# Kernel tuning notes

Measured on AMD Instinct MI355X. Metric: run time of the kernel, lower is better.

## Reference

```python
import jax, jax.numpy as jnp
import numpy as np

# Clebsch-Gordan coefficients in the real basis; l=1 components stored in (y,z,x) order
S2 = 1.0 / np.sqrt(2.0)
S3 = 1.0 / np.sqrt(3.0)
S6 = 1.0 / np.sqrt(6.0)
_C2 = np.zeros((5, 3, 3), np.float32)
_C2[0, 2, 0] = _C2[0, 0, 2] = S2          # ~ xy
_C2[1, 0, 1] = _C2[1, 1, 0] = S2          # ~ yz
_C2[2, 1, 1] = 2.0 * S6                   # ~ 2z^2 - x^2 - y^2
_C2[2, 2, 2] = -S6
_C2[2, 0, 0] = -S6
_C2[3, 2, 1] = _C2[3, 1, 2] = S2          # ~ xz
_C2[4, 2, 2] = S2                          # ~ x^2 - y^2
_C2[4, 0, 0] = -S2
C2 = jnp.asarray(_C2)

N0, N1 = 64, 32        # multiplicities of input 0e / 1o irreps
CUTOFF = 5.0


def basis_functions(pos):
    """pos [N,3] -> (scalars [N,64], l=1 features [N,32,3])."""
    r = jnp.linalg.norm(pos, axis=-1, keepdims=True) + 1e-9        # [N,1]
    d = pos[:, (1, 2, 0)] / r                                       # unit dir, (y,z,x) order
    c0 = jnp.linspace(0.0, CUTOFF, N0, dtype=pos.dtype)
    c1 = jnp.linspace(0.0, CUTOFF, N1, dtype=pos.dtype)
    f0 = jnp.exp(-4.0 * (r - c0) ** 2)                              # [N,64] gaussian RBF
    f1 = jnp.exp(-4.0 * (r - c1) ** 2)                              # [N,32]
    x1 = f1[:, :, None] * d[:, None, :]                             # [N,32,3]
    return f0, x1


def lin_l(x, W):
    # channel mixing within one irrep block; preserves the m axis if present
    if x.ndim == 2:
        return x @ W
    return jnp.einsum('ncm,cd->ndm', x, W)


def tensor_product(a0, a1, b0, b1):
    """Full uvw CG tensor product of (64x0 + 32x1) x (64x0 + 32x1)."""
    N = a0.shape[0]
    # l=0 outputs: 0x0->0 and 1x1->0
    p000 = jnp.einsum('na,nb->nab', a0, b0).reshape(N, -1)                 # [N,4096]
    p110 = jnp.einsum('nam,nbm->nab', a1, b1).reshape(N, -1) * S3          # [N,1024]
    t0 = jnp.concatenate([p000, p110], axis=1)                             # [N,5120]
    # l=1 outputs: 0x1->1, 1x0->1, 1x1->1 (cross product)
    p011 = (a0[:, :, None, None] * b1[:, None, :, :]).reshape(N, -1, 3)    # [N,2048,3]
    p101 = (a1[:, :, None, :] * b0[:, None, :, None]).reshape(N, -1, 3)    # [N,2048,3]
    p111 = (jnp.cross(a1[:, :, None, :], b1[:, None, :, :]) * S2).reshape(N, -1, 3)
    t1 = jnp.concatenate([p011, p101, p111], axis=1)                       # [N,5120,3]
    # l=2 output: 1x1->2 via CG tensor
    t2 = jnp.einsum('nai,nbj,mij->nabm', a1, b1, C2).reshape(N, -1, 5)     # [N,1024,5]
    return t0, t1, t2


def setup_inputs() -> dict:
    key = jax.random.key(0)
    ks = jax.random.split(key, 10)
    N = 4096
    def w(k, i, o):
        return jax.random.normal(k, (i, o), jnp.float32) / np.sqrt(i)
    return {
        'positions': jax.random.normal(ks[0], (N, 3), jnp.float32) * 2.0,
        'W1_0': w(ks[1], 64, 64),
        'W1_1': w(ks[2], 32, 32),
        'W2_0': w(ks[3], 64, 64),
        'W2_1': w(ks[4], 32, 32),
        'W3_0': w(ks[5], 5120, 64),
        'W3_1': w(ks[6], 5120, 32),
        'W3_2': w(ks[7], 1024, 16),
        'W_out': w(ks[8], 240, 7),
        'b_out': jnp.zeros((7,), jnp.float32),
    }


def reference(positions, W1_0, W1_1, W2_0, W2_1, W3_0, W3_1, W3_2, W_out, b_out):
    f0, f1 = basis_functions(positions)                 # 64x0, 32x1
    a0, a1 = lin_l(f0, W1_0), lin_l(f1, W1_1)           # linear1
    b0, b1 = lin_l(f0, W2_0), lin_l(f1, W2_1)           # linear2
    t0, t1, t2 = tensor_product(a0, a1, b0, b1)         # 5120x0, 5120x1, 1024x2
    y0 = lin_l(t0, W3_0)                                # [N,64]
    y1 = lin_l(t1, W3_1)                                # [N,32,3]
    y2 = lin_l(t2, W3_2)                                # [N,16,5]
    N = y0.shape[0]
    feat = jnp.concatenate([y0, y1.reshape(N, -1), y2.reshape(N, -1)], axis=1)  # [N,240]
    return feat @ W_out + b_out                         # [N,7]
```

## Files before the change

### kernel.cpp

```cpp
#include <hip/hip_runtime.h>
#include <math.h>

#define NS2 0.70710678118654752440f
#define NS3 0.57735026918962576451f
#define NS6 0.40824829046386301636f

typedef _Float16 f16;
typedef _Float16 f16x8 __attribute__((ext_vector_type(8)));
typedef float    f32x4 __attribute__((ext_vector_type(4)));

#define GT_K    22528
#define UV_ROW  216
#define OFF_UV  157696

__global__ __launch_bounds__(256) void prep_kernel(
    const float* __restrict__ pos,
    const float* __restrict__ W1_0, const float* __restrict__ W1_1,
    const float* __restrict__ W2_0, const float* __restrict__ W2_1,
    const float* __restrict__ W3_0, const float* __restrict__ W3_1,
    const float* __restrict__ W3_2, const float* __restrict__ Wout,
    const float* __restrict__ bout,
    f16* __restrict__ wsh, float* __restrict__ out, int N)
{
    __shared__ float smem[3728];
    const int tid = threadIdx.x;

    if (blockIdx.x < 352) {
        float* s_wo  = smem;
        float* s_red = smem + 1680;
        for (int i = tid; i < 1680; i += 256) s_wo[i] = Wout[i];
        __syncthreads();
        const int kl = tid & 63, q = tid >> 6;
        const int k  = blockIdx.x * 64 + kl;
        float acc[7] = {0.f,0.f,0.f,0.f,0.f,0.f,0.f};
        if (k < 4096) {
            const float* wr = W3_0 + (size_t)k * 64;
            #pragma unroll
            for (int oo = 0; oo < 16; oo += 4) {
                int o = q*16 + oo;
                float4 wv = *(const float4*)(wr + o);
                const float* w0 = s_wo + o * 7;
                #pragma unroll
                for (int kk = 0; kk < 7; ++kk)
                    acc[kk] = fmaf(wv.x, w0[kk], fmaf(wv.y, w0[7+kk],
                              fmaf(wv.z, w0[14+kk], fmaf(wv.w, w0[21+kk], acc[kk]))));
            }
        } else if (k < 10240) {
            int it = k >> 6, s = it - 64, m = s >> 5, a2 = s & 31, l = k & 63;
            const float* wr = W3_1 + (size_t)(2048 + a2*64 + l) * 32;
            #pragma unroll
            for (int oo = 0; oo < 8; oo += 4) {
                int o = q*8 + oo;
                float4 wv = *(const float4*)(wr + o);
                const float* w0 = s_wo + (64 + o*3 + m) * 7;
                #pragma unroll
                for (int kk = 0; kk < 7; ++kk)
                    acc[kk] = fmaf(wv.x, w0[kk], fmaf(wv.y, w0[21+kk],
                              fmaf(wv.z, w0[42+kk], fmaf(wv.w, w0[63+kk], acc[kk]))));
            }
        } else {
            int it2 = (k - 10240) >> 5, l32 = k & 31;
            if (it2 < 32) {
                const float* wr = W3_0 + (size_t)(4096 + it2*32 + l32) * 64;
                #pragma unroll
                for (int oo = 0; oo < 16; oo += 4) {
                    int o = q*16 + oo;
                    float4 wv = *(const float4*)(wr + o);
                    const float* w0 = s_wo + o * 7;
                    #pragma unroll
                    for (int kk = 0; kk < 7; ++kk)
                        acc[kk] = fmaf(wv.x, w0[kk], fmaf(wv.y, w0[7+kk],
                                  fmaf(wv.z, w0[14+kk], fmaf(wv.w, w0[21+kk], acc[kk]))));
                }
            } else if (it2 < 224) {
                int t = it2 - 32, m = t >> 6, a = t & 63;
                const float* wr = W3_1 + (size_t)(a*32 + l32) * 32;
                #pragma unroll
                for (int oo = 0; oo < 8; oo += 4) {
                    int o = q*8 + oo;
                    float4 wv = *(const float4*)(wr + o);
                    const float* w0 = s_wo + (64 + o*3 + m) * 7;
                    #pragma unroll
                    for (int kk = 0; kk < 7; ++kk)
                        acc[kk] = fmaf(wv.x, w0[kk], fmaf(wv.y, w0[21+kk],
                                  fmaf(wv.z, w0[42+kk], fmaf(wv.w, w0[63+kk], acc[kk]))));
                }
            } else {
                int t = it2 - 224, m = t >> 5, a = t & 31;
                const float* wr = W3_2 + (size_t)(a*32 + l32) * 16;
                int o = q*4;
                float4 wv = *(const float4*)(wr + o);
                const float* w0 = s_wo + (160 + o*5 + m) * 7;
                #pragma unroll
                for (int kk = 0; kk < 7; ++kk)
                    acc[kk] = fmaf(wv.x, w0[kk], fmaf(wv.y, w0[35+kk],
                              fmaf(wv.z, w0[70+kk], fmaf(wv.w, w0[105+kk], acc[kk]))));
            }
        }
        #pragma unroll
        for (int r = 0; r < 7; ++r) s_red[(q*64 + kl)*8 + r] = acc[r];
        __syncthreads();
        if (tid < 64) {
            #pragma unroll
            for (int r = 0; r < 7; ++r) {
                float v = s_red[(      tid)*8 + r] + s_red[( 64 + tid)*8 + r]
                        + s_red[(128 + tid)*8 + r] + s_red[(192 + tid)*8 + r];
                wsh[(size_t)r * GT_K + blockIdx.x*64 + tid] = (f16)v;
            }
        }
        return;
    }

    float* s_f0 = smem;
    float* s_f1 = smem + 512;
    const int g8   = blockIdx.x - 352;
    const int base = g8 * 8;
    f16* uv = wsh + OFF_UV;
    {
        int d = tid & 63;
        #pragma unroll
        for (int jj = 0; jj < 2; ++jj) {
            int j = (tid >> 6) + jj * 4;
            int n = base + j;
            float px = pos[n*3+0], py = pos[n*3+1], pz = pos[n*3+2];
            float r  = sqrtf(px*px + py*py + pz*pz) + 1e-9f;
            float t0 = r - (5.0f/63.0f) * (float)d;
            s_f0[j*64 + d] = __expf(-4.f * t0 * t0);
        }
        {
            int j = tid >> 5, d1 = tid & 31;
            int n = base + j;
            float px = pos[n*3+0], py = pos[n*3+1], pz = pos[n*3+2];
            float r  = sqrtf(px*px + py*py + pz*pz) + 1e-9f;
            float t1 = r - (5.0f/31.0f) * (float)d1;
            s_f1[j*32 + d1] = __expf(-4.f * t1 * t1);
        }
        if (tid < 8) {
            int n = base + tid;
            float px = pos[n*3+0], py = pos[n*3+1], pz = pos[n*3+2];
            float r  = sqrtf(px*px + py*py + pz*pz) + 1e-9f;
            float iv = 1.0f / r;
            float d0 = py*iv, d1 = pz*iv, d2 = px*iv;
            f16* row = uv + (size_t)n * UV_ROW;
            row[192+0] = (f16)d0;
            row[192+1] = (f16)d1;
            row[192+2] = (f16)d2;
            row[192+3] = (f16)(NS3 * (d0*d0 + d1*d1 + d2*d2));
            row[192+4] = (f16)(2.f*NS2*d2*d0);
            row[192+5] = (f16)(2.f*NS2*d0*d1);
            row[192+6] = (f16)(NS6*(2.f*d1*d1 - d2*d2 - d0*d0));
            row[192+7] = (f16)(2.f*NS2*d2*d1);
            row[192+8] = (f16)(NS2*(d2*d2 - d0*d0));
            row[201]   = (f16)1.0f;
        }
        if (tid < 56) out[base*7 + tid] = bout[tid % 7];
    }
    __syncthreads();
    {
        int c = tid & 63, jb = tid >> 6;
        float aa0 = 0.f, aa1 = 0.f, ba0 = 0.f, ba1 = 0.f;
        const float* wa = W1_0 + c;
        const float* wb = W2_0 + c;
        #pragma unroll 4
        for (int d = 0; d < 64; ++d) {
            float wav = wa[d*64], wbv = wb[d*64];
            float fA = s_f0[jb*64 + d], fB = s_f0[(jb+4)*64 + d];
            aa0 = fmaf(fA, wav, aa0);  aa1 = fmaf(fB, wav, aa1);
            ba0 = fmaf(fA, wbv, ba0);  ba1 = fmaf(fB, wbv, ba1);
        }
        uv[(size_t)(base+jb  )*UV_ROW +      c] = (f16)aa0;
        uv[(size_t)(base+jb+4)*UV_ROW +      c] = (f16)aa1;
        uv[(size_t)(base+jb  )*UV_ROW + 96 + c] = (f16)ba0;
        uv[(size_t)(base+jb+4)*UV_ROW + 96 + c] = (f16)ba1;

        int c1 = tid & 31, j8 = tid >> 5;
        float aA = 0.f, aB = 0.f;
        const float* wA = W1_1 + c1;
        const float* wB = W2_1 + c1;
        #pragma unroll 4
        for (int d = 0; d < 32; ++d) {
            float f = s_f1[j8*32 + d];
            aA = fmaf(f, wA[d*32], aA);
            aB = fmaf(f, wB[d*32], aB);
        }
        uv[(size_t)(base+j8)*UV_ROW +  64 + c1] = (f16)aA;
        uv[(size_t)(base+j8)*UV_ROW + 160 + c1] = (f16)aB;
    }
}

__global__ __launch_bounds__(256) void main_kernel(
    const f16* __restrict__ wsh, float* __restrict__ out, int N)
{
    __shared__ f16 s_g[2][8][264];
    __shared__ f16 s_uv[64][UV_ROW];
    __shared__ f16 s_ugt[2][64][8];
    __shared__ unsigned short s_idx[704];

    const int tid  = threadIdx.x;
    const int w    = tid >> 6;
    const int lane = tid & 63;
    const int lq   = lane >> 4;
    const int lm   = lane & 15;
    const int ra   = (lm < 7) ? lm : 7;
    const int g    = blockIdx.x >> 3;
    const int kq   = blockIdx.x & 7;

    {
        const uint4* src = (const uint4*)(wsh + OFF_UV + (size_t)g * 64 * UV_ROW);
        uint4* dst = (uint4*)&s_uv[0][0];
        for (int j = tid; j < 1728; j += 256) dst[j] = src[j];
        for (int c = tid; c < 704; c += 256) {
            int uidx, gidx;
            if (c < 320) {
                int it = c >> 1;
                if (it < 64) { uidx = it; gidx = 9; }
                else { int s = it - 64; uidx = 64 + (s & 31); gidx = s >> 5; }
            } else {
                int it2 = c - 320;
                if (it2 < 32)       { uidx = 64 + it2;                 gidx = 3; }
                else if (it2 < 224) { int t = it2 - 32;  uidx = t & 63;        gidx = t >> 6; }
                else                { int t = it2 - 224; uidx = 64 + (t & 31); gidx = 4 + (t >> 5); }
            }
            s_idx[c] = (unsigned short)(uidx | (gidx << 8));
        }
        for (int i = tid; i < 264; i += 256) {
            s_g[0][7][i] = (f16)0.f;
            s_g[1][7][i] = (f16)0.f;
        }
    }
    __syncthreads();

    const f16* myrow = &s_uv[w*16 + lm][0];
    f16x8 vA0 = *(const f16x8*)(myrow +  96 + lq*8);
    f16x8 vA1 = *(const f16x8*)(myrow + 128 + lq*8);
    f16x8 vB  = *(const f16x8*)(myrow + 160 + lq*8);

    auto c0_of = [&](int t) {
        return (t < 5) ? (kq*40 + t*8) : (320 + kq*48 + (t-5)*8);
    };
    auto stage = [&](int t, int buf) {
        int c0 = c0_of(t), k0 = c0 * 32;
        const f16* src = wsh + k0;
        for (int j = tid; j < 224; j += 256) {
            int row = j >> 5, col = j & 31;
            uint4 v = *(const uint4*)(src + (size_t)row * GT_K + col*8);
            *(uint4*)&s_g[buf][row][col*8] = v;
        }
        for (int j = tid; j < 512; j += 256) {
            int n = j >> 3, s = j & 7;
            unsigned short ix = s_idx[c0 + s];
            float u  = (float)s_uv[n][ix & 255];
            float gg = (float)s_uv[n][192 + (ix >> 8)];
            s_ugt[buf][n][s] = (f16)(u * gg);
        }
    };

    f32x4 acc = {0.f, 0.f, 0.f, 0.f};
    auto compute = [&](int buf, bool isA) {
        #pragma unroll
        for (int s = 0; s < 8; ++s) {
            f16x8 a = *(const f16x8*)&s_g[buf][ra][s*32 + lq*8];
            f16 ug  = s_ugt[buf][w*16 + lm][s];
            f16x8 vv = isA ? ((s & 1) ? vA1 : vA0) : vB;
            f16x8 b;
            #pragma unroll
            for (int j2 = 0; j2 < 8; ++j2) b[j2] = vv[j2] * ug;
            acc = __builtin_amdgcn_mfma_f32_16x16x32_f16(a, b, acc, 0, 0, 0);
        }
    };

    stage(0, 0);
    __syncthreads();
    for (int t = 0; t < 11; ++t) {
        int buf = t & 1;
        if (t < 10) stage(t + 1, buf ^ 1);
        compute(buf, t < 5);
        __syncthreads();
    }

    int node = g*64 + w*16 + lm;
    if (lq == 0) {
        #pragma unroll
        for (int r = 0; r < 4; ++r) atomicAdd(&out[node*7 + r], acc[r]);
    } else if (lq == 1) {
        #pragma unroll
        for (int r = 0; r < 3; ++r) atomicAdd(&out[node*7 + 4 + r], acc[r]);
    }
}

extern "C" void kernel_launch(void* const* d_in, const int* in_sizes, int n_in,
                              void* d_out, int out_size, void* d_ws, size_t ws_size,
                              hipStream_t stream)
{
    const float* pos  = (const float*)d_in[0];
    const float* W1_0 = (const float*)d_in[1];
    const float* W1_1 = (const float*)d_in[2];
    const float* W2_0 = (const float*)d_in[3];
    const float* W2_1 = (const float*)d_in[4];
    const float* W3_0 = (const float*)d_in[5];
    const float* W3_1 = (const float*)d_in[6];
    const float* W3_2 = (const float*)d_in[7];
    const float* Wout = (const float*)d_in[8];
    const float* bout = (const float*)d_in[9];
    f16*   wsh = (f16*)d_ws;
    float* op  = (float*)d_out;
    int N = in_sizes[0] / 3;

    prep_kernel<<<352 + N/8, 256, 0, stream>>>(pos, W1_0, W1_1, W2_0, W2_1,
                                               W3_0, W3_1, W3_2, Wout, bout, wsh, op, N);
    main_kernel<<<512, 256, 0, stream>>>(wsh, op, N);
}
```

Measured before the change: 97.84 us.

## Fuse prep and main kernels via cooperative grid sync, prefetch staging into registers

Merges the weight-folding and node-feature prep phase with the MFMA contraction phase into one cooperative kernel of 512 blocks. Each block builds 44 GT columns and 8 nodes, then a grid-wide sync precedes the main phase, removing one kernel launch and the gap between launches. The staging of GT tiles is split so the global load is issued before compute and the shared-memory store happens after it, overlapping load latency with MFMA work. The per-row scale vector is also read as one 8-wide load. If the cooperative launch fails, it falls back to the original two-kernel path. Grid sync costs and the mapping of 512x44 onto GT_K columns must fit exactly.

```diff
diff --git a/kernel.cpp b/kernel.cpp
--- a/kernel.cpp
+++ b/kernel.cpp
@@ -1,4 +1,5 @@
 #include <hip/hip_runtime.h>
+#include <hip/hip_cooperative_groups.h>
 #include <math.h>
 
 #define NS2 0.70710678118654752440f
@@ -13,25 +14,21 @@
 #define UV_ROW  216
 #define OFF_UV  157696
 
-__global__ __launch_bounds__(256) void prep_kernel(
-    const float* __restrict__ pos,
-    const float* __restrict__ W1_0, const float* __restrict__ W1_1,
-    const float* __restrict__ W2_0, const float* __restrict__ W2_1,
+namespace cg = cooperative_groups;
+
+__device__ __forceinline__ void build_gt(
     const float* __restrict__ W3_0, const float* __restrict__ W3_1,
     const float* __restrict__ W3_2, const float* __restrict__ Wout,
-    const float* __restrict__ bout,
-    f16* __restrict__ wsh, float* __restrict__ out, int N)
-{
-    __shared__ float smem[3728];
+    f16* __restrict__ wsh, float* smem, int k_base, int n_k)
+{
     const int tid = threadIdx.x;
-
-    if (blockIdx.x < 352) {
-        float* s_wo  = smem;
-        float* s_red = smem + 1680;
-        for (int i = tid; i < 1680; i += 256) s_wo[i] = Wout[i];
-        __syncthreads();
-        const int kl = tid & 63, q = tid >> 6;
-        const int k  = blockIdx.x * 64 + kl;
+    float* s_wo  = smem;
+    float* s_red = smem + 1680;
+    for (int i = tid; i < 1680; i += 256) s_wo[i] = Wout[i];
+    __syncthreads();
+    const int kl = tid & 63, q = tid >> 6;
+    if (kl < n_k) {
+        const int k = k_base + kl;
         float acc[7] = {0.f,0.f,0.f,0.f,0.f,0.f,0.f};
         if (k < 4096) {
             const float* wr = W3_0 + (size_t)k * 64;
@@ -99,22 +96,28 @@
         }
         #pragma unroll
         for (int r = 0; r < 7; ++r) s_red[(q*64 + kl)*8 + r] = acc[r];
-        __syncthreads();
-        if (tid < 64) {
-            #pragma unroll
-            for (int r = 0; r < 7; ++r) {
-                float v = s_red[(      tid)*8 + r] + s_red[( 64 + tid)*8 + r]
-                        + s_red[(128 + tid)*8 + r] + s_red[(192 + tid)*8 + r];
-                wsh[(size_t)r * GT_K + blockIdx.x*64 + tid] = (f16)v;
-            }
-        }
-        return;
-    }
-
+    }
+    __syncthreads();
+    if (tid < n_k) {
+        #pragma unroll
+        for (int r = 0; r < 7; ++r) {
+            float v = s_red[(      tid)*8 + r] + s_red[( 64 + tid)*8 + r]
+                    + s_red[(128 + tid)*8 + r] + s_red[(192 + tid)*8 + r];
+            wsh[(size_t)r * GT_K + k_base + tid] = (f16)v;
+        }
+    }
+}
+
+__device__ __forceinline__ void build_nodes(
+    const float* __restrict__ pos,
+    const float* __restrict__ W1_0, const float* __restrict__ W1_1,
+    const float* __restrict__ W2_0, const float* __restrict__ W2_1,
+    const float* __restrict__ bout,
+    f16* __restrict__ wsh, float* __restrict__ out, float* smem, int base)
+{
+    const int tid = threadIdx.x;
     float* s_f0 = smem;
     float* s_f1 = smem + 512;
-    const int g8   = blockIdx.x - 352;
-    const int base = g8 * 8;
     f16* uv = wsh + OFF_UV;
     {
         int d = tid & 63;
@@ -188,13 +191,14 @@
     }
 }
 
-__global__ __launch_bounds__(256) void main_kernel(
-    const f16* __restrict__ wsh, float* __restrict__ out, int N)
-{
-    __shared__ f16 s_g[2][8][264];
-    __shared__ f16 s_uv[64][UV_ROW];
-    __shared__ f16 s_ugt[2][64][8];
-    __shared__ unsigned short s_idx[704];
+__device__ __forceinline__ void phaseB(const f16* __restrict__ wsh,
+                                       float* __restrict__ out,
+                                       char* smem_raw, int g, int kq)
+{
+    f16 (*s_g)[8][264]   = (f16(*)[8][264])(smem_raw);
+    f16 (*s_uv)[UV_ROW]  = (f16(*)[UV_ROW])(smem_raw + 8448);
+    f16 (*s_ugt)[64][8]  = (f16(*)[64][8])(smem_raw + 8448 + 27648);
+    unsigned short* s_idx = (unsigned short*)(smem_raw + 8448 + 27648 + 2048);
 
     const int tid  = threadIdx.x;
     const int w    = tid >> 6;
@@ -202,8 +206,6 @@
     const int lq   = lane >> 4;
     const int lm   = lane & 15;
     const int ra   = (lm < 7) ? lm : 7;
-    const int g    = blockIdx.x >> 3;
-    const int kq   = blockIdx.x & 7;
 
     {
         const uint4* src = (const uint4*)(wsh + OFF_UV + (size_t)g * 64 * UV_ROW);
@@ -238,15 +240,17 @@
     auto c0_of = [&](int t) {
         return (t < 5) ? (kq*40 + t*8) : (320 + kq*48 + (t-5)*8);
     };
-    auto stage = [&](int t, int buf) {
-        int c0 = c0_of(t), k0 = c0 * 32;
-        const f16* src = wsh + k0;
-        for (int j = tid; j < 224; j += 256) {
-            int row = j >> 5, col = j & 31;
-            uint4 v = *(const uint4*)(src + (size_t)row * GT_K + col*8);
-            *(uint4*)&s_g[buf][row][col*8] = v;
-        }
-        for (int j = tid; j < 512; j += 256) {
+
+    const int  srow  = tid >> 5, scol = tid & 31;
+    const bool shave = tid < 224;
+    uint4 gv;
+    auto stage_pre = [&](int t, int buf) {
+        int c0 = c0_of(t);
+        if (shave)
+            gv = *(const uint4*)(wsh + c0*32 + (size_t)srow * GT_K + scol*8);
+        #pragma unroll
+        for (int rep = 0; rep < 2; ++rep) {
+            int j = tid + rep*256;
             int n = j >> 3, s = j & 7;
             unsigned short ix = s_idx[c0 + s];
             float u  = (float)s_uv[n][ix & 255];
@@ -254,13 +258,17 @@
             s_ugt[buf][n][s] = (f16)(u * gg);
         }
     };
+    auto stage_post = [&](int buf) {
+        if (shave) *(uint4*)&s_g[buf][srow][scol*8] = gv;
+    };
 
     f32x4 acc = {0.f, 0.f, 0.f, 0.f};
     auto compute = [&](int buf, bool isA) {
+        const f16x8 ug8 = *(const f16x8*)&s_ugt[buf][w*16 + lm][0];
         #pragma unroll
         for (int s = 0; s < 8; ++s) {
             f16x8 a = *(const f16x8*)&s_g[buf][ra][s*32 + lq*8];
-            f16 ug  = s_ugt[buf][w*16 + lm][s];
+            f16 ug  = ug8[s];
             f16x8 vv = isA ? ((s & 1) ? vA1 : vA0) : vB;
             f16x8 b;
             #pragma unroll
@@ -269,12 +277,13 @@
         }
     };
 
-    stage(0, 0);
+    stage_pre(0, 0); stage_post(0);
     __syncthreads();
     for (int t = 0; t < 11; ++t) {
         int buf = t & 1;
-        if (t < 10) stage(t + 1, buf ^ 1);
+        if (t < 10) stage_pre(t + 1, buf ^ 1);
         compute(buf, t < 5);
+        if (t < 10) stage_post(buf ^ 1);
         __syncthreads();
     }
 
@@ -286,6 +295,54 @@
         #pragma unroll
         for (int r = 0; r < 3; ++r) atomicAdd(&out[node*7 + 4 + r], acc[r]);
     }
+}
+
+__global__ __launch_bounds__(256, 2) void fused_kernel(
+    const float* __restrict__ pos,
+    const float* __restrict__ W1_0, const float* __restrict__ W1_1,
+    const float* __restrict__ W2_0, const float* __restrict__ W2_1,
+    const float* __restrict__ W3_0, const float* __restrict__ W3_1,
+    const float* __restrict__ W3_2, const float* __restrict__ Wout,
+    const float* __restrict__ bout,
+    f16* __restrict__ wsh, float* __restrict__ out, int N)
+{
+    __shared__ __align__(16) char smem_raw[39552];
+    (void)N;
+
+    build_gt(W3_0, W3_1, W3_2, Wout, wsh, (float*)smem_raw, blockIdx.x * 44, 44);
+    build_nodes(pos, W1_0, W1_1, W2_0, W2_1, bout, wsh, out,
+                (float*)smem_raw, blockIdx.x * 8);
+
+    __threadfence();
+    cg::this_grid().sync();
+
+    phaseB(wsh, out, smem_raw, blockIdx.x >> 3, blockIdx.x & 7);
+}
+
+__global__ __launch_bounds__(256) void prep_kernel(
+    const float* __restrict__ pos,
+    const float* __restrict__ W1_0, const float* __restrict__ W1_1,
+    const float* __restrict__ W2_0, const float* __restrict__ W2_1,
+    const float* __restrict__ W3_0, const float* __restrict__ W3_1,
+    const float* __restrict__ W3_2, const float* __restrict__ Wout,
+    const float* __restrict__ bout,
+    f16* __restrict__ wsh, float* __restrict__ out, int N)
+{
+    __shared__ __align__(16) float smem[3728];
+    (void)N;
+    if (blockIdx.x < 352)
+        build_gt(W3_0, W3_1, W3_2, Wout, wsh, smem, blockIdx.x * 64, 64);
+    else
+        build_nodes(pos, W1_0, W1_1, W2_0, W2_1, bout, wsh, out, smem,
+                    (blockIdx.x - 352) * 8);
+}
+
+__global__ __launch_bounds__(256) void main_kernel(
+    const f16* __restrict__ wsh, float* __restrict__ out, int N)
+{
+    __shared__ __align__(16) char smem_raw[39552];
+    (void)N;
+    phaseB(wsh, out, smem_raw, blockIdx.x >> 3, blockIdx.x & 7);
 }
 
 extern "C" void kernel_launch(void* const* d_in, const int* in_sizes, int n_in,
@@ -306,7 +363,18 @@
     float* op  = (float*)d_out;
     int N = in_sizes[0] / 3;
 
-    prep_kernel<<<352 + N/8, 256, 0, stream>>>(pos, W1_0, W1_1, W2_0, W2_1,
-                                               W3_0, W3_1, W3_2, Wout, bout, wsh, op, N);
-    main_kernel<<<512, 256, 0, stream>>>(wsh, op, N);
-}
+    void* args[] = { (void*)&pos, (void*)&W1_0, (void*)&W1_1, (void*)&W2_0,
+                     (void*)&W2_1, (void*)&W3_0, (void*)&W3_1, (void*)&W3_2,
+                     (void*)&Wout, (void*)&bout, (void*)&wsh, (void*)&op,
+                     (void*)&N };
+    hipError_t e = hipLaunchCooperativeKernel((void*)fused_kernel,
+                                              dim3(512), dim3(256),
+                                              args, 0, stream);
+    if (e != hipSuccess) {
+        (void)hipGetLastError();
+        prep_kernel<<<352 + N/8, 256, 0, stream>>>(pos, W1_0, W1_1, W2_0, W2_1,
+                                                   W3_0, W3_1, W3_2, Wout, bout,
+                                                   wsh, op, N);
+        main_kernel<<<512, 256, 0, stream>>>(wsh, op, N);
+    }
+}
```

After: 180.0 us. +84.0%, slower.

## Load full weight slice into LDS upfront and rebalance prep kernel blocks

Applied to the files above, without the earlier changes.

The main kernel no longer runs an 11-step double-buffered staging loop with a barrier each step. It now loads the whole per-block slice of the folded weight matrix and the node features into registers, writes them to a single large shared buffer, and precomputes all u*g scale factors once before an unrolled MFMA loop. The loop uses two accumulators to break the MFMA dependency chain. The prep kernel is restructured so every block does both a weight-folding chunk of 44 rows and an 8-node feature chunk, which evens out work across 512 blocks. The trade-off is about 79KB of LDS per block, which can limit occupancy, plus higher register pressure.

```diff
diff --git a/kernel.cpp b/kernel.cpp
--- a/kernel.cpp
+++ b/kernel.cpp
@@ -13,25 +13,19 @@
 #define UV_ROW  216
 #define OFF_UV  157696
 
-__global__ __launch_bounds__(256) void prep_kernel(
-    const float* __restrict__ pos,
-    const float* __restrict__ W1_0, const float* __restrict__ W1_1,
-    const float* __restrict__ W2_0, const float* __restrict__ W2_1,
+__device__ __forceinline__ void build_gt(
     const float* __restrict__ W3_0, const float* __restrict__ W3_1,
     const float* __restrict__ W3_2, const float* __restrict__ Wout,
-    const float* __restrict__ bout,
-    f16* __restrict__ wsh, float* __restrict__ out, int N)
-{
-    __shared__ float smem[3728];
+    f16* __restrict__ wsh, float* smem, int k_base, int n_k)
+{
     const int tid = threadIdx.x;
-
-    if (blockIdx.x < 352) {
-        float* s_wo  = smem;
-        float* s_red = smem + 1680;
-        for (int i = tid; i < 1680; i += 256) s_wo[i] = Wout[i];
-        __syncthreads();
-        const int kl = tid & 63, q = tid >> 6;
-        const int k  = blockIdx.x * 64 + kl;
+    float* s_wo  = smem;
+    float* s_red = smem + 1680;
+    for (int i = tid; i < 1680; i += 256) s_wo[i] = Wout[i];
+    __syncthreads();
+    const int kl = tid & 63, q = tid >> 6;
+    if (kl < n_k) {
+        const int k = k_base + kl;
         float acc[7] = {0.f,0.f,0.f,0.f,0.f,0.f,0.f};
         if (k < 4096) {
             const float* wr = W3_0 + (size_t)k * 64;
@@ -99,22 +93,28 @@
         }
         #pragma unroll
         for (int r = 0; r < 7; ++r) s_red[(q*64 + kl)*8 + r] = acc[r];
-        __syncthreads();
-        if (tid < 64) {
-            #pragma unroll
-            for (int r = 0; r < 7; ++r) {
-                float v = s_red[(      tid)*8 + r] + s_red[( 64 + tid)*8 + r]
-                        + s_red[(128 + tid)*8 + r] + s_red[(192 + tid)*8 + r];
-                wsh[(size_t)r * GT_K + blockIdx.x*64 + tid] = (f16)v;
-            }
-        }
-        return;
-    }
-
+    }
+    __syncthreads();
+    if (tid < n_k) {
+        #pragma unroll
+        for (int r = 0; r < 7; ++r) {
+            float v = s_red[(      tid)*8 + r] + s_red[( 64 + tid)*8 + r]
+                    + s_red[(128 + tid)*8 + r] + s_red[(192 + tid)*8 + r];
+            wsh[(size_t)r * GT_K + k_base + tid] = (f16)v;
+        }
+    }
+}
+
+__device__ __forceinline__ void build_nodes(
+    const float* __restrict__ pos,
+    const float* __restrict__ W1_0, const float* __restrict__ W1_1,
+    const float* __restrict__ W2_0, const float* __restrict__ W2_1,
+    const float* __restrict__ bout,
+    f16* __restrict__ wsh, float* __restrict__ out, float* smem, int base)
+{
+    const int tid = threadIdx.x;
     float* s_f0 = smem;
     float* s_f1 = smem + 512;
-    const int g8   = blockIdx.x - 352;
-    const int base = g8 * 8;
     f16* uv = wsh + OFF_UV;
     {
         int d = tid & 63;
@@ -188,103 +188,153 @@
     }
 }
 
+__global__ __launch_bounds__(256) void prep_kernel(
+    const float* __restrict__ pos,
+    const float* __restrict__ W1_0, const float* __restrict__ W1_1,
+    const float* __restrict__ W2_0, const float* __restrict__ W2_1,
+    const float* __restrict__ W3_0, const float* __restrict__ W3_1,
+    const float* __restrict__ W3_2, const float* __restrict__ Wout,
+    const float* __restrict__ bout,
+    f16* __restrict__ wsh, float* __restrict__ out, int N)
+{
+    __shared__ __align__(16) float smem[3728];
+    (void)N;
+    build_gt(W3_0, W3_1, W3_2, Wout, wsh, smem, blockIdx.x * 44, 44);
+    build_nodes(pos, W1_0, W1_1, W2_0, W2_1, bout, wsh, out, smem,
+                blockIdx.x * 8);
+}
+
 __global__ __launch_bounds__(256) void main_kernel(
     const f16* __restrict__ wsh, float* __restrict__ out, int N)
 {
-    __shared__ f16 s_g[2][8][264];
-    __shared__ f16 s_uv[64][UV_ROW];
-    __shared__ f16 s_ugt[2][64][8];
-    __shared__ unsigned short s_idx[704];
+    __shared__ __align__(16) char smem[79248];
+    f16* s_g   = (f16*)smem;
+    f16* s_uv  = (f16*)(smem + 39648);
+    f16* s_ugt = (f16*)(smem + 67296);
+    unsigned short* s_idx = (unsigned short*)(smem + 79072);
+    (void)N;
 
     const int tid  = threadIdx.x;
     const int w    = tid >> 6;
     const int lane = tid & 63;
     const int lq   = lane >> 4;
     const int lm   = lane & 15;
-    const int ra   = (lm < 7) ? lm : 7;
+    const int ra   = lm % 7;
     const int g    = blockIdx.x >> 3;
     const int kq   = blockIdx.x & 7;
 
+    uint4 ru[7];
     {
         const uint4* src = (const uint4*)(wsh + OFF_UV + (size_t)g * 64 * UV_ROW);
-        uint4* dst = (uint4*)&s_uv[0][0];
-        for (int j = tid; j < 1728; j += 256) dst[j] = src[j];
-        for (int c = tid; c < 704; c += 256) {
-            int uidx, gidx;
-            if (c < 320) {
-                int it = c >> 1;
-                if (it < 64) { uidx = it; gidx = 9; }
-                else { int s = it - 64; uidx = 64 + (s & 31); gidx = s >> 5; }
-            } else {
-                int it2 = c - 320;
-                if (it2 < 32)       { uidx = 64 + it2;                 gidx = 3; }
-                else if (it2 < 224) { int t = it2 - 32;  uidx = t & 63;        gidx = t >> 6; }
-                else                { int t = it2 - 224; uidx = 64 + (t & 31); gidx = 4 + (t >> 5); }
-            }
-            s_idx[c] = (unsigned short)(uidx | (gidx << 8));
-        }
-        for (int i = tid; i < 264; i += 256) {
-            s_g[0][7][i] = (f16)0.f;
-            s_g[1][7][i] = (f16)0.f;
-        }
-    }
-    __syncthreads();
-
-    const f16* myrow = &s_uv[w*16 + lm][0];
+        #pragma unroll
+        for (int it = 0; it < 7; ++it) {
+            int j = tid + it*256;
+            if (j < 1728) ru[it] = src[j];
+        }
+    }
+    uint4 rg[10];
+    #pragma unroll
+    for (int it = 0; it < 10; ++it) {
+        int j = tid + it*256;
+        if (j < 2464) {
+            int row = j / 352, col = j - row*352;
+            size_t off = (size_t)row * GT_K +
+                         (col < 160 ? kq*1280 + col*8
+                                    : 10240 + kq*1536 + (col-160)*8);
+            rg[it] = *(const uint4*)(wsh + off);
+        }
+    }
+    if (tid < 88) {
+        int c  = tid;
+        int gc = (c < 40) ? (kq*40 + c) : (320 + kq*48 + (c - 40));
+        int uidx, gidx;
+        if (gc < 320) {
+            int it = gc >> 1;
+            if (it < 64) { uidx = it; gidx = 9; }
+            else { int s = it - 64; uidx = 64 + (s & 31); gidx = s >> 5; }
+        } else {
+            int it2 = gc - 320;
+            if (it2 < 32)       { uidx = 64 + it2;                  gidx = 3; }
+            else if (it2 < 224) { int t = it2 - 32;  uidx = t & 63;         gidx = t >> 6; }
+            else                { int t = it2 - 224; uidx = 64 + (t & 31);  gidx = 4 + (t >> 5); }
+        }
+        s_idx[c] = (unsigned short)(uidx | (gidx << 8));
+    }
+    {
+        uint4* dst = (uint4*)s_uv;
+        #pragma unroll
+        for (int it = 0; it < 7; ++it) {
+            int j = tid + it*256;
+            if (j < 1728) dst[j] = ru[it];
+        }
+    }
+    #pragma unroll
+    for (int it = 0; it < 10; ++it) {
+        int j = tid + it*256;
+        if (j < 2464) {
+            int row = j / 352, col = j - row*352;
+            *(uint4*)(s_g + row*2832 + col*8) = rg[it];
+        }
+    }
+    __syncthreads();
+
+    #pragma unroll
+    for (int it = 0; it < 22; ++it) {
+        int j = tid + it*256;
+        int n = j / 88, c = j - n*88;
+        unsigned short ix = s_idx[c];
+        float u  = (float)s_uv[n*UV_ROW + (ix & 255)];
+        float gg = (float)s_uv[n*UV_ROW + 192 + (ix >> 8)];
+        s_ugt[n*92 + c] = (f16)(u * gg);
+    }
+    const f16* myrow = s_uv + (w*16 + lm) * UV_ROW;
     f16x8 vA0 = *(const f16x8*)(myrow +  96 + lq*8);
     f16x8 vA1 = *(const f16x8*)(myrow + 128 + lq*8);
     f16x8 vB  = *(const f16x8*)(myrow + 160 + lq*8);
-
-    auto c0_of = [&](int t) {
-        return (t < 5) ? (kq*40 + t*8) : (320 + kq*48 + (t-5)*8);
-    };
-    auto stage = [&](int t, int buf) {
-        int c0 = c0_of(t), k0 = c0 * 32;
-        const f16* src = wsh + k0;
-        for (int j = tid; j < 224; j += 256) {
-            int row = j >> 5, col = j & 31;
-            uint4 v = *(const uint4*)(src + (size_t)row * GT_K + col*8);
-            *(uint4*)&s_g[buf][row][col*8] = v;
-        }
-        for (int j = tid; j < 512; j += 256) {
-            int n = j >> 3, s = j & 7;
-            unsigned short ix = s_idx[c0 + s];
-            float u  = (float)s_uv[n][ix & 255];
-            float gg = (float)s_uv[n][192 + (ix >> 8)];
-            s_ugt[buf][n][s] = (f16)(u * gg);
-        }
-    };
-
-    f32x4 acc = {0.f, 0.f, 0.f, 0.f};
-    auto compute = [&](int buf, bool isA) {
+    __syncthreads();
+
+    f32x4 acc0 = {0.f,0.f,0.f,0.f}, acc1 = {0.f,0.f,0.f,0.f};
+    const f16* arow  = s_g + ra*2832 + lq*8;
+    const f16* ugrow = s_ugt + (w*16 + lm)*92;
+    #pragma unroll
+    for (int cb = 0; cb < 5; ++cb) {
+        f16x8 ug8 = *(const f16x8*)(ugrow + cb*8);
         #pragma unroll
         for (int s = 0; s < 8; ++s) {
-            f16x8 a = *(const f16x8*)&s_g[buf][ra][s*32 + lq*8];
-            f16 ug  = s_ugt[buf][w*16 + lm][s];
-            f16x8 vv = isA ? ((s & 1) ? vA1 : vA0) : vB;
+            int c = cb*8 + s;
+            f16x8 a  = *(const f16x8*)(arow + c*32);
+            f16x8 vv = (s & 1) ? vA1 : vA0;
+            f16 ug   = ug8[s];
             f16x8 b;
             #pragma unroll
             for (int j2 = 0; j2 < 8; ++j2) b[j2] = vv[j2] * ug;
-            acc = __builtin_amdgcn_mfma_f32_16x16x32_f16(a, b, acc, 0, 0, 0);
-        }
-    };
-
-    stage(0, 0);
-    __syncthreads();
-    for (int t = 0; t < 11; ++t) {
-        int buf = t & 1;
-        if (t < 10) stage(t + 1, buf ^ 1);
-        compute(buf, t < 5);
-        __syncthreads();
+            if (s & 1) acc1 = __builtin_amdgcn_mfma_f32_16x16x32_f16(a, b, acc1, 0, 0, 0);
+            else       acc0 = __builtin_amdgcn_mfma_f32_16x16x32_f16(a, b, acc0, 0, 0, 0);
+        }
+    }
+    #pragma unroll
+    for (int cb = 5; cb < 11; ++cb) {
+        f16x8 ug8 = *(const f16x8*)(ugrow + cb*8);
+        #pragma unroll
+        for (int s = 0; s < 8; ++s) {
+            int c = cb*8 + s;
+            f16x8 a  = *(const f16x8*)(arow + c*32);
+            f16 ug   = ug8[s];
+            f16x8 b;
+            #pragma unroll
+            for (int j2 = 0; j2 < 8; ++j2) b[j2] = vB[j2] * ug;
+            if (s & 1) acc1 = __builtin_amdgcn_mfma_f32_16x16x32_f16(a, b, acc1, 0, 0, 0);
+            else       acc0 = __builtin_amdgcn_mfma_f32_16x16x32_f16(a, b, acc0, 0, 0, 0);
+        }
     }
 
     int node = g*64 + w*16 + lm;
     if (lq == 0) {
         #pragma unroll
-        for (int r = 0; r < 4; ++r) atomicAdd(&out[node*7 + r], acc[r]);
+        for (int r = 0; r < 4; ++r) atomicAdd(&out[node*7 + r], acc0[r] + acc1[r]);
     } else if (lq == 1) {
         #pragma unroll
-        for (int r = 0; r < 3; ++r) atomicAdd(&out[node*7 + 4 + r], acc[r]);
+        for (int r = 0; r < 3; ++r) atomicAdd(&out[node*7 + 4 + r], acc0[r] + acc1[r]);
     }
 }
 
@@ -306,7 +356,7 @@
     float* op  = (float*)d_out;
     int N = in_sizes[0] / 3;
 
-    prep_kernel<<<352 + N/8, 256, 0, stream>>>(pos, W1_0, W1_1, W2_0, W2_1,
-                                               W3_0, W3_1, W3_2, Wout, bout, wsh, op, N);
+    prep_kernel<<<512, 256, 0, stream>>>(pos, W1_0, W1_1, W2_0, W2_1,
+                                         W3_0, W3_1, W3_2, Wout, bout, wsh, op, N);
     main_kernel<<<512, 256, 0, stream>>>(wsh, op, N);
 }
```

After: 104.8 us. 7.1% more time.
